# Kernel tuning notes

Measured on AMD Instinct MI355X. Metric: run time of the kernel, lower is better.

## Reference

```python
import jax, jax.numpy as jnp
import numpy as np

STRIDE = 16
A = 9
PRE_NMS_TOP_N = 6000
POST_NMS_TOP_N = 300
NMS_THRESH = 0.7
MIN_SIZE = 16
H, W = 128, 192


def _generate_anchors(base_size=16, ratios=(0.5, 1.0, 2.0), scales=(8, 16, 32)):
    base = np.array([0, 0, base_size - 1, base_size - 1], dtype=np.float64)
    w = base[2] - base[0] + 1
    h = base[3] - base[1] + 1
    x_ctr = base[0] + 0.5 * (w - 1)
    y_ctr = base[1] + 0.5 * (h - 1)
    size = w * h
    ratios = np.array(ratios)
    ws = np.round(np.sqrt(size / ratios))
    hs = np.round(ws * ratios)
    ratio_anchors = np.stack([x_ctr - 0.5 * (ws - 1), y_ctr - 0.5 * (hs - 1),
                              x_ctr + 0.5 * (ws - 1), y_ctr + 0.5 * (hs - 1)], axis=1)
    out = []
    scales = np.array(scales)
    for a in ratio_anchors:
        aw = a[2] - a[0] + 1
        ah = a[3] - a[1] + 1
        xc = a[0] + 0.5 * (aw - 1)
        yc = a[1] + 0.5 * (ah - 1)
        ws2 = aw * scales
        hs2 = ah * scales
        out.append(np.stack([xc - 0.5 * (ws2 - 1), yc - 0.5 * (hs2 - 1),
                             xc + 0.5 * (ws2 - 1), yc + 0.5 * (hs2 - 1)], axis=1))
    return np.concatenate(out, axis=0).astype(np.float32)  # [9,4]


def setup_inputs() -> dict:
    key = jax.random.key(0)
    k1, k2 = jax.random.split(key)
    scores = jax.random.uniform(k1, (1, 2 * A, H, W), dtype=jnp.float32)
    bbox_deltas = 0.1 * jax.random.normal(k2, (1, 4 * A, H, W), dtype=jnp.float32)
    im_info = jnp.array([[H * STRIDE, W * STRIDE, 1.0]], dtype=jnp.float32)
    return {"scores": scores, "bbox_deltas": bbox_deltas, "im_info": im_info}


def _proposal_forward(scores, bbox_deltas, im_info):
    anchors_base = jnp.asarray(_generate_anchors())  # [A,4]
    sc = scores[:, A:, :, :]                          # fg scores [1,A,H,W]
    h, w = sc.shape[-2], sc.shape[-1]
    shift_x = (jnp.arange(w) * STRIDE).astype(sc.dtype)
    shift_y = (jnp.arange(h) * STRIDE).astype(sc.dtype)
    sy, sx = jnp.meshgrid(shift_y, shift_x, indexing='ij')
    shifts = jnp.stack([sx.ravel(), sy.ravel(), sx.ravel(), sy.ravel()], axis=1)  # [K,4]
    anchors = (anchors_base[None, :, :] + shifts[:, None, :]).reshape(-1, 4)      # [K*A,4]

    deltas = bbox_deltas.transpose(0, 2, 3, 1).reshape(-1, 4)
    deltas = jnp.concatenate([deltas[:, :2], jnp.clip(deltas[:, 2:], -10.0, 10.0)], axis=1)
    sc = sc.transpose(0, 2, 3, 1).reshape(-1)  # [K*A]

    widths = anchors[:, 2] - anchors[:, 0] + 1.0
    heights = anchors[:, 3] - anchors[:, 1] + 1.0
    ctr_x = anchors[:, 0] + 0.5 * widths
    ctr_y = anchors[:, 1] + 0.5 * heights
    dx, dy, dw, dh = deltas[:, 0], deltas[:, 1], deltas[:, 2], deltas[:, 3]
    pcx = dx * widths + ctr_x
    pcy = dy * heights + ctr_y
    pw = jnp.exp(dw) * widths
    ph = jnp.exp(dh) * heights
    x1 = pcx - 0.5 * pw
    y1 = pcy - 0.5 * ph
    x2 = pcx + 0.5 * pw
    y2 = pcy + 0.5 * ph

    info = im_info[0]
    x1 = jnp.clip(x1, 0.0, info[1] - 1.0)
    x2 = jnp.clip(x2, 0.0, info[1] - 1.0)
    y1 = jnp.clip(y1, 0.0, info[0] - 1.0)
    y2 = jnp.clip(y2, 0.0, info[0] - 1.0)
    proposals = jnp.stack([x1, y1, x2, y2], axis=1)

    # filter_boxes: mask (instead of dropping) boxes smaller than min_size*scale
    min_sz = MIN_SIZE * info[2]
    valid = ((x2 - x1 + 1.0) >= min_sz) & ((y2 - y1 + 1.0) >= min_sz)
    masked = jnp.where(valid, sc, -jnp.inf)

    # sort desc + pre_nms_topN
    top_scores, top_idx = jax.lax.top_k(masked, PRE_NMS_TOP_N)
    boxes = proposals[top_idx]               # [PRE,4], score-descending
    tvalid = top_scores > -jnp.inf

    # pairwise IoU (torchvision convention)
    area = (boxes[:, 2] - boxes[:, 0]) * (boxes[:, 3] - boxes[:, 1])
    lt = jnp.maximum(boxes[:, None, :2], boxes[None, :, :2])
    rb = jnp.minimum(boxes[:, None, 2:], boxes[None, :, 2:])
    wh = jnp.clip(rb - lt, 0.0)
    inter = wh[..., 0] * wh[..., 1]
    iou = inter / (area[:, None] + area[None, :] - inter)  # [PRE,PRE]

    # greedy NMS over score-sorted boxes
    n = PRE_NMS_TOP_N
    def step(keep, x):
        iou_col, v, i = x
        suppressed = jnp.any(keep & (iou_col > NMS_THRESH))
        k = v & jnp.logical_not(suppressed)
        keep = keep.at[i].set(k)
        return keep, k
    keep, _ = jax.lax.scan(step, jnp.zeros((n,), dtype=bool),
                           (iou.T, tvalid, jnp.arange(n)))

    # kept boxes first (stable => score order preserved), take post_nms_topN
    order = jnp.argsort(jnp.logical_not(keep).astype(jnp.int32), stable=True)[:POST_NMS_TOP_N]
    kept = keep[order]
    out_boxes = jnp.where(kept[:, None], boxes[order], 0.0)
    output = jnp.concatenate(
        [jnp.zeros((POST_NMS_TOP_N, 1), out_boxes.dtype), out_boxes], axis=1)
    return output  # [POST,5]: (batch_idx=0, x1,y1,x2,y2); rows beyond kept count are zero


def reference(scores, bbox_deltas, im_info):
    return _proposal_forward(scores, bbox_deltas, im_info)
```

## Files before the change

### kernel.cpp

```cpp
#include <hip/hip_runtime.h>

#define N_ANCH 221184
#define HW     24576
#define Wd     192
#define AA     9
#define TOPN   6000
#define POSTN  300
#define CAND_CAP 8192
#define NWORDS 94
#define NCHUNK 47

typedef unsigned long long u64;

__device__ const float c_aw[9] = {184.f,368.f,736.f,128.f,256.f,512.f, 88.f,176.f,352.f};
__device__ const float c_ah[9] = { 96.f,192.f,384.f,128.f,256.f,512.f,176.f,352.f,704.f};

__device__ __forceinline__ float4 decode_box(int a, int cell,
                                             const float* __restrict__ deltas,
                                             float info0, float info1, float info2,
                                             bool* valid) {
    int h = cell / Wd;
    int w = cell - h * Wd;
    const float* db = deltas + (size_t)(4 * a) * HW + cell;
    float dx = db[0];
    float dy = db[HW];
    float dw = db[2 * HW];
    float dh = db[3 * HW];
    dw = fminf(fmaxf(dw, -10.f), 10.f);
    dh = fminf(fmaxf(dh, -10.f), 10.f);

    float ww = c_aw[a], hh = c_ah[a];
    float cx = 16.f * (float)w + 8.f;
    float cy = 16.f * (float)h + 8.f;

    float pcx = __fadd_rn(__fmul_rn(dx, ww), cx);
    float pcy = __fadd_rn(__fmul_rn(dy, hh), cy);
    float pw  = __fmul_rn(expf(dw), ww);
    float ph  = __fmul_rn(expf(dh), hh);
    float hpw = __fmul_rn(0.5f, pw);
    float hph = __fmul_rn(0.5f, ph);
    float x1 = __fsub_rn(pcx, hpw);
    float x2 = __fadd_rn(pcx, hpw);
    float y1 = __fsub_rn(pcy, hph);
    float y2 = __fadd_rn(pcy, hph);

    float xmax = __fsub_rn(info1, 1.f);
    float ymax = __fsub_rn(info0, 1.f);
    x1 = fminf(fmaxf(x1, 0.f), xmax);
    x2 = fminf(fmaxf(x2, 0.f), xmax);
    y1 = fminf(fmaxf(y1, 0.f), ymax);
    y2 = fminf(fmaxf(y2, 0.f), ymax);

    float msz = __fmul_rn(16.f, info2);
    *valid = (__fadd_rn(__fsub_rn(x2, x1), 1.f) >= msz) &&
             (__fadd_rn(__fsub_rn(y2, y1), 1.f) >= msz);
    return make_float4(x1, y1, x2, y2);
}

#define ZA_F4 4164
#define ZB_F4 48
__global__ __launch_bounds__(256) void init_kernel(float4* zA, float4* zB) {
    int t = blockIdx.x * 256 + threadIdx.x;
    float4 z = make_float4(0.f, 0.f, 0.f, 0.f);
    if (t < ZA_F4) zA[t] = z;
    else if (t < ZA_F4 + ZB_F4) zB[t - ZA_F4] = z;
}

__global__ __launch_bounds__(256) void decode_kernel(const float* __restrict__ scores,
                                                     const float* __restrict__ deltas,
                                                     const float* __restrict__ iminfo,
                                                     unsigned int* __restrict__ keys,
                                                     unsigned int* __restrict__ hist256) {
    __shared__ unsigned int lh[256];
    lh[threadIdx.x] = 0u;
    __syncthreads();
    int t = blockIdx.x * 256 + threadIdx.x;
    int a = t / HW;
    int cell = t - a * HW;
    float score = scores[(AA + a) * HW + cell];
    bool valid;
    (void)decode_box(a, cell, deltas, iminfo[0], iminfo[1], iminfo[2], &valid);
    unsigned int sb = __float_as_uint(score);
    unsigned int key = valid ? ((sb & 0x80000000u) ? ~sb : (sb | 0x80000000u))
                             : 0x007FFFFFu;
    keys[t] = key;
    atomicAdd(&lh[key >> 24], 1u);
    __syncthreads();
    if (lh[threadIdx.x]) atomicAdd(&hist256[threadIdx.x], lh[threadIdx.x]);
}

__global__ __launch_bounds__(1024) void midselect_kernel(const unsigned int* __restrict__ keys,
                                                         const unsigned int* __restrict__ hist256,
                                                         unsigned int* __restrict__ state) {
    __shared__ unsigned int sfx[256];
    __shared__ unsigned int h2w[16][256];
    __shared__ unsigned int sP, sRank;
    int t = threadIdx.x;
    int wv = t >> 6;
    for (int i = t; i < 16 * 256; i += 1024) ((unsigned int*)h2w)[i] = 0u;
    if (t < 256) sfx[t] = hist256[t];
    __syncthreads();
    for (int d = 1; d < 256; d <<= 1) {
        unsigned int v = 0u;
        if (t < 256 && t + d < 256) v = sfx[t + d];
        __syncthreads();
        if (t < 256) sfx[t] += v;
        __syncthreads();
    }
    if (t < 256) {
        unsigned int ge = sfx[t];
        unsigned int gt = (t < 255) ? sfx[t + 1] : 0u;
        if (ge >= TOPN && gt < TOPN) { sP = (unsigned int)t; sRank = TOPN - gt; }
    }
    __syncthreads();
    unsigned int P = sP, rank = sRank;
    const uint4* k4 = (const uint4*)keys;
    for (int i = t; i < N_ANCH / 4; i += 1024) {
        uint4 v = k4[i];
        if ((v.x >> 24) == P) atomicAdd(&h2w[wv][(v.x >> 16) & 0xFFu], 1u);
        if ((v.y >> 24) == P) atomicAdd(&h2w[wv][(v.y >> 16) & 0xFFu], 1u);
        if ((v.z >> 24) == P) atomicAdd(&h2w[wv][(v.z >> 16) & 0xFFu], 1u);
        if ((v.w >> 24) == P) atomicAdd(&h2w[wv][(v.w >> 16) & 0xFFu], 1u);
    }
    __syncthreads();
    if (t < 256) {
        unsigned int s = 0;
        #pragma unroll
        for (int wvi = 0; wvi < 16; ++wvi) s += h2w[wvi][t];
        sfx[t] = s;
    }
    __syncthreads();
    for (int d = 1; d < 256; d <<= 1) {
        unsigned int v = 0u;
        if (t < 256 && t + d < 256) v = sfx[t + d];
        __syncthreads();
        if (t < 256) sfx[t] += v;
        __syncthreads();
    }
    if (t < 256) {
        unsigned int ge = sfx[t];
        unsigned int gt = (t < 255) ? sfx[t + 1] : 0u;
        if (ge >= rank && gt < rank) {
            state[0] = (P << 24) | ((unsigned int)t << 16);
            state[2] = 0u;
        }
    }
}

__global__ __launch_bounds__(256) void compact_kernel(const unsigned int* __restrict__ keys,
                                                      unsigned int* __restrict__ state,
                                                      u64* __restrict__ cand) {
    int t = blockIdx.x * 256 + threadIdx.x;
    unsigned int k = keys[t];
    unsigned int T = state[0];
    if (k >= T) {
        unsigned int pos = atomicAdd(&state[2], 1u);
        if (pos < CAND_CAP) {
            int a = t / HW;
            int cell = t - a * HW;
            unsigned int aidx = (unsigned int)(cell * 9 + a);
            cand[pos] = ((u64)k << 32) | (u64)(~aidx);
        }
    }
}

__global__ __launch_bounds__(256) void rank_scatter_kernel(const u64* __restrict__ cand,
                                                           const float* __restrict__ deltas,
                                                           const float* __restrict__ iminfo,
                                                           float4* __restrict__ tb,
                                                           u64* __restrict__ vmask) {
    __shared__ u64 s[CAND_CAP];
    for (int j = threadIdx.x; j < CAND_CAP; j += 256) s[j] = cand[j];
    int part = threadIdx.x & 7;
    int i = blockIdx.x * 32 + (threadIdx.x >> 3);
    u64 k = cand[i];
    __syncthreads();
    const ulonglong2* sv = (const ulonglong2*)s;
    unsigned int cnt = 0;
    #pragma unroll 8
    for (int jj = part; jj < CAND_CAP / 2; jj += 8) {
        ulonglong2 v = sv[jj];
        cnt += (v.x > k) ? 1u : 0u;
        cnt += (v.y > k) ? 1u : 0u;
    }
    cnt += __shfl_xor(cnt, 1);
    cnt += __shfl_xor(cnt, 2);
    cnt += __shfl_xor(cnt, 4);
    if (part == 0 && k != 0ull && cnt < TOPN) {
        unsigned int aidx = ~((unsigned int)k);
        int a = (int)(aidx % 9u);
        int cell = (int)(aidx / 9u);
        bool valid;
        float4 box = decode_box(a, cell, deltas, iminfo[0], iminfo[1], iminfo[2], &valid);
        tb[cnt] = box;
        if ((unsigned int)(k >> 32) != 0x007FFFFFu)
            atomicOr(&vmask[cnt >> 6], 1ull << (cnt & 63));
    }
}

__global__ __launch_bounds__(64) void nms_matrix_kernel(const float4* __restrict__ tb,
                                                        u64* __restrict__ mat) {
    if (blockIdx.x < blockIdx.y) return;
    __shared__ float4 cb[64];
    int t = threadIdx.x;
    int c0 = blockIdx.x * 64;
    int col = c0 + t;
    cb[t] = (col < TOPN) ? tb[col] : make_float4(0.f, 0.f, 0.f, 0.f);
    __syncthreads();
    int row = blockIdx.y * 64 + t;
    if (row >= TOPN) return;
    float4 rb = tb[row];
    float rA = (rb.z - rb.x) * (rb.w - rb.y);
    u64 mask = 0ull;
    for (int c = 0; c < 64; ++c) {
        if (c0 + c >= TOPN) break;
        float4 b = cb[c];
        float lx = fmaxf(rb.x, b.x), ly = fmaxf(rb.y, b.y);
        float rx = fminf(rb.z, b.z), ry = fminf(rb.w, b.w);
        float iw = fmaxf(rx - lx, 0.f), ih = fmaxf(ry - ly, 0.f);
        float inter = iw * ih;
        float bA = (b.z - b.x) * (b.w - b.y);
        float iou = inter / ((rA + bA) - inter);
        if (iou > 0.7f) mask |= (1ull << c);
    }
    mat[(size_t)row * NWORDS + blockIdx.x] = mask;
}

__device__ __forceinline__ u64 rdl64(u64 v, int l) {
    unsigned int lo = (unsigned int)__builtin_amdgcn_readlane((int)(unsigned int)v, l);
    unsigned int hi = (unsigned int)__builtin_amdgcn_readlane((int)(unsigned int)(v >> 32), l);
    return ((u64)hi << 32) | (u64)lo;
}

__global__ __launch_bounds__(64) void nms_scan_kernel(const u64* __restrict__ mat,
                                                      const u64* __restrict__ vmask,
                                                      const float4* __restrict__ tb,
                                                      float* __restrict__ out) {
    int lane = threadIdx.x;
    u64 r0 = ~vmask[lane];
    u64 r1 = (lane < NWORDS - 64) ? ~vmask[64 + lane] : ~0ull;
    __shared__ int kept[POSTN];
    int cnt = 0;

    u64 a0, a1, b0, b1;
    {
        ulonglong2 vA = *(const ulonglong2*)(mat + (size_t)lane * NWORDS);
        ulonglong2 vB = *(const ulonglong2*)(mat + (size_t)(64 + lane) * NWORDS);
        a0 = vA.x; a1 = vA.y; b0 = vB.x; b1 = vB.y;
    }
    for (int c = 0; c < NCHUNK; ++c) {
        u64 na0 = 0, na1 = 0, nb0 = 0, nb1 = 0;
        if (c + 1 < NCHUNK) {
            const u64* pA = mat + (size_t)((c + 1) * 128 + lane) * NWORDS + 2 * (c + 1);
            const u64* pB = mat + (size_t)((c + 1) * 128 + 64 + lane) * NWORDS + 2 * (c + 1);
            ulonglong2 vA = *(const ulonglong2*)pA;
            ulonglong2 vB = *(const ulonglong2*)pB;
            na0 = vA.x; na1 = vA.y; nb0 = vB.x; nb1 = vB.y;
        }
        int w2 = 2 * c;
        u64 s0 = (w2 < 64) ? rdl64(r0, w2) : rdl64(r1, w2 - 64);
        u64 s1 = (w2 + 1 < 64) ? rdl64(r0, w2 + 1) : rdl64(r1, w2 + 1 - 64);
        if ((s0 & s1) != ~0ull) {
            int base = c * 128;
            u64 rem0 = s0, rem1 = s1, k0 = 0ull, k1 = 0ull;
            while (cnt < POSTN) {
                int b;
                if (~rem0) b = __ffsll((u64)~rem0) - 1;
                else if (~rem1) b = 64 + __ffsll((u64)~rem1) - 1;
                else break;
                if (lane == 0) kept[cnt] = base + b;
                ++cnt;
                u64 w0, w1;
                if (b < 64) {
                    w0 = rdl64(a0, b); w1 = rdl64(a1, b);
                    k0 |= 1ull << b; rem0 |= 1ull << b;
                } else {
                    int bb = b - 64;
                    w0 = rdl64(b0, bb); w1 = rdl64(b1, bb);
                    k1 |= 1ull << bb; rem1 |= 1ull << bb;
                }
                rem0 |= w0; rem1 |= w1;
            }
            if (cnt >= POSTN) break;
            u64 f0 = 0ull, f1 = 0ull, m0 = k0, m1 = k1;
            while (m0 | m1) {
                int idxs[8];
                #pragma unroll
                for (int j = 0; j < 8; ++j) {
                    int b = -1;
                    if (m0) { b = __ffsll(m0) - 1; m0 &= m0 - 1; }
                    else if (m1) { b = 64 + __ffsll(m1) - 1; m1 &= m1 - 1; }
                    idxs[j] = b;
                }
                u64 v0[8], v1[8];
                #pragma unroll
                for (int j = 0; j < 8; ++j) {
                    v0[j] = 0ull; v1[j] = 0ull;
                    if (idxs[j] >= 0) {
                        const u64* row = mat + (size_t)(base + idxs[j]) * NWORDS;
                        v0[j] = row[lane];
                        if (lane < NWORDS - 64) v1[j] = row[64 + lane];
                    }
                }
                #pragma unroll
                for (int j = 0; j < 8; ++j) { f0 |= v0[j]; f1 |= v1[j]; }
            }
            r0 |= f0; r1 |= f1;
        }
        a0 = na0; a1 = na1; b0 = nb0; b1 = nb1;
    }

    for (int r = lane; r < POSTN; r += 64) {
        float4 b = make_float4(0.f, 0.f, 0.f, 0.f);
        if (r < cnt) b = tb[kept[r]];
        float* o = out + r * 5;
        o[0] = 0.f; o[1] = b.x; o[2] = b.y; o[3] = b.z; o[4] = b.w;
    }
}

extern "C" void kernel_launch(void* const* d_in, const int* in_sizes, int n_in,
                              void* d_out, int out_size, void* d_ws, size_t ws_size,
                              hipStream_t stream) {
    const float* scores = (const float*)d_in[0];
    const float* deltas = (const float*)d_in[1];
    const float* iminfo = (const float*)d_in[2];
    float* out = (float*)d_out;

    char* ws = (char*)d_ws;
    unsigned int* keys    = (unsigned int*)(ws + 0);
    unsigned int* hist256 = (unsigned int*)(ws + 884736);
    unsigned int* state   = (unsigned int*)(ws + 885760);
    u64*          cand    = (u64*)(ws + 885824);
    float4*       tb      = (float4*)(ws + 951360);
    u64*          vmask   = (u64*)(ws + 1047616);
    u64*          mat     = (u64*)(ws + 1048384);

    const int NB = N_ANCH / 256;

    init_kernel<<<17, 256, 0, stream>>>((float4*)hist256, (float4*)vmask);
    decode_kernel<<<NB, 256, 0, stream>>>(scores, deltas, iminfo, keys, hist256);
    midselect_kernel<<<1, 1024, 0, stream>>>(keys, hist256, state);
    compact_kernel<<<NB, 256, 0, stream>>>(keys, state, cand);
    rank_scatter_kernel<<<CAND_CAP / 32, 256, 0, stream>>>(cand, deltas, iminfo, tb, vmask);
    nms_matrix_kernel<<<dim3(NWORDS, NWORDS), 64, 0, stream>>>(tb, mat);
    nms_scan_kernel<<<1, 64, 0, stream>>>(mat, vmask, tb, out);
}
```

Before: 249.1 us.

## Speculatively prefetch next chunk's suppression rows and deepen diagonal-block prefetch

The serial NMS scan now prefetches the diagonal mask blocks four chunks ahead instead of one. While processing a chunk, it also speculatively loads up to eight mask rows for the next chunk's currently-unsuppressed candidates, so the dependent global loads overlap with the current chunk's work. When the kept boxes of a chunk match the speculated rows, the prefetched data is reused and only uncovered rows are fetched. This costs extra register pressure and some wasted loads when speculation misses, in exchange for hiding memory latency on the single-wavefront critical path.

```diff
diff --git a/kernel.cpp b/kernel.cpp
--- a/kernel.cpp
+++ b/kernel.cpp
@@ -232,6 +232,126 @@
     return ((u64)hi << 32) | (u64)lo;
 }
 
+struct Spec {
+    u64 v0[8];
+    u64 v1[8];
+    u64 m0, m1;
+};
+
+__device__ __forceinline__ bool chunk_body(int c, int lane,
+                                           const u64* __restrict__ mat,
+                                           ulonglong2 dA, ulonglong2 dB,
+                                           Spec& in, Spec& out,
+                                           u64& r0, u64& r1, int& cnt,
+                                           int* kept) {
+    const int w2 = 2 * c;
+    u64 s0 = (w2 < 64) ? rdl64(r0, w2) : rdl64(r1, w2 - 64);
+    u64 s1 = (w2 + 1 < 64) ? rdl64(r0, w2 + 1) : rdl64(r1, w2 + 1 - 64);
+
+    {
+        const int cn = (c + 1 < NCHUNK) ? (c + 1) : (NCHUNK - 1);
+        const int w2n = 2 * cn;
+        u64 t0 = (w2n < 64) ? rdl64(r0, w2n) : rdl64(r1, w2n - 64);
+        u64 t1 = (w2n + 1 < 64) ? rdl64(r0, w2n + 1) : rdl64(r1, w2n + 1 - 64);
+        u64 p0 = ~t0, p1 = ~t1;
+        out.m0 = p0; out.m1 = p1;
+        const int nbase = cn * 128;
+        const u64 lmask = (lane < NWORDS - 64) ? ~0ull : 0ull;
+        const int l1 = (lane < NWORDS - 64) ? (64 + lane) : 63;
+        u64 mm0 = p0, mm1 = p1;
+        #pragma unroll
+        for (int j = 0; j < 8; ++j) {
+            int b = -1;
+            if (mm0)      { b = __ffsll(mm0) - 1;      mm0 &= mm0 - 1; }
+            else if (mm1) { b = 64 + __ffsll(mm1) - 1; mm1 &= mm1 - 1; }
+            int bS = (b >= 0) ? b : 0;
+            const u64* row = mat + (size_t)(nbase + bS) * NWORDS;
+            u64 x0 = row[lane];
+            u64 x1 = row[l1];
+            u64 live = (b >= 0) ? ~0ull : 0ull;
+            out.v0[j] = x0 & live;
+            out.v1[j] = x1 & live & lmask;
+        }
+    }
+
+    if ((s0 & s1) != ~0ull) {
+        const int base = c * 128;
+        u64 rem0 = s0, rem1 = s1, k0 = 0ull, k1 = 0ull;
+        while (cnt < POSTN) {
+            int b;
+            if (~rem0)      b = __ffsll((u64)~rem0) - 1;
+            else if (~rem1) b = 64 + __ffsll((u64)~rem1) - 1;
+            else break;
+            if (lane == 0) kept[cnt] = base + b;
+            ++cnt;
+            if (b < 64) {
+                rem0 |= rdl64(dA.x, b);
+                rem1 |= rdl64(dA.y, b);
+                k0 |= 1ull << b; rem0 |= 1ull << b;
+            } else {
+                int bb = b - 64;
+                rem0 |= rdl64(dB.x, bb);
+                rem1 |= rdl64(dB.y, bb);
+                k1 |= 1ull << bb; rem1 |= 1ull << bb;
+            }
+        }
+        if (cnt >= POSTN) return true;
+
+        if (k0 | k1) {
+            u64 mm0 = in.m0, mm1 = in.m1, cov0 = 0ull, cov1 = 0ull;
+            u64 f0 = 0ull, f1 = 0ull;
+            #pragma unroll
+            for (int j = 0; j < 8; ++j) {
+                int b = -1;
+                if (mm0)      { b = __ffsll(mm0) - 1;      mm0 &= mm0 - 1; }
+                else if (mm1) { b = 64 + __ffsll(mm1) - 1; mm1 &= mm1 - 1; }
+                if (b >= 0) {
+                    u64 kj;
+                    if (b < 64) { kj = (k0 >> b) & 1ull;        cov0 |= 1ull << b; }
+                    else        { kj = (k1 >> (b - 64)) & 1ull; cov1 |= 1ull << (b - 64); }
+                    u64 msk = 0ull - kj;
+                    f0 |= in.v0[j] & msk;
+                    f1 |= in.v1[j] & msk;
+                }
+            }
+            u64 lk0 = k0 & ~cov0, lk1 = k1 & ~cov1;
+            if (lk0 | lk1) {
+                u64 m0 = lk0, m1 = lk1;
+                while (m0 | m1) {
+                    int idxs[8];
+                    #pragma unroll
+                    for (int j = 0; j < 8; ++j) {
+                        int b = -1;
+                        if (m0)      { b = __ffsll(m0) - 1;      m0 &= m0 - 1; }
+                        else if (m1) { b = 64 + __ffsll(m1) - 1; m1 &= m1 - 1; }
+                        idxs[j] = b;
+                    }
+                    u64 v0[8], v1[8];
+                    #pragma unroll
+                    for (int j = 0; j < 8; ++j) {
+                        v0[j] = 0ull; v1[j] = 0ull;
+                        if (idxs[j] >= 0) {
+                            const u64* row = mat + (size_t)(base + idxs[j]) * NWORDS;
+                            v0[j] = row[lane];
+                            if (lane < NWORDS - 64) v1[j] = row[64 + lane];
+                        }
+                    }
+                    #pragma unroll
+                    for (int j = 0; j < 8; ++j) { f0 |= v0[j]; f1 |= v1[j]; }
+                }
+            }
+            r0 |= f0; r1 |= f1;
+        }
+    }
+    return false;
+}
+
+#define LDIAG(cc, A, B) do {                                                  \
+    int c_ = (cc) < NCHUNK ? (cc) : (NCHUNK - 1);                             \
+    const u64* pA_ = mat + (size_t)(c_ * 128 + lane) * NWORDS + 2 * c_;       \
+    const u64* pB_ = mat + (size_t)(c_ * 128 + 64 + lane) * NWORDS + 2 * c_;  \
+    A = *(const ulonglong2*)pA_; B = *(const ulonglong2*)pB_; } while (0)
+
 __global__ __launch_bounds__(64) void nms_scan_kernel(const u64* __restrict__ mat,
                                                       const u64* __restrict__ vmask,
                                                       const float4* __restrict__ tb,
@@ -242,72 +362,34 @@
     __shared__ int kept[POSTN];
     int cnt = 0;
 
-    u64 a0, a1, b0, b1;
-    {
-        ulonglong2 vA = *(const ulonglong2*)(mat + (size_t)lane * NWORDS);
-        ulonglong2 vB = *(const ulonglong2*)(mat + (size_t)(64 + lane) * NWORDS);
-        a0 = vA.x; a1 = vA.y; b0 = vB.x; b1 = vB.y;
-    }
-    for (int c = 0; c < NCHUNK; ++c) {
-        u64 na0 = 0, na1 = 0, nb0 = 0, nb1 = 0;
-        if (c + 1 < NCHUNK) {
-            const u64* pA = mat + (size_t)((c + 1) * 128 + lane) * NWORDS + 2 * (c + 1);
-            const u64* pB = mat + (size_t)((c + 1) * 128 + 64 + lane) * NWORDS + 2 * (c + 1);
-            ulonglong2 vA = *(const ulonglong2*)pA;
-            ulonglong2 vB = *(const ulonglong2*)pB;
-            na0 = vA.x; na1 = vA.y; nb0 = vB.x; nb1 = vB.y;
-        }
-        int w2 = 2 * c;
-        u64 s0 = (w2 < 64) ? rdl64(r0, w2) : rdl64(r1, w2 - 64);
-        u64 s1 = (w2 + 1 < 64) ? rdl64(r0, w2 + 1) : rdl64(r1, w2 + 1 - 64);
-        if ((s0 & s1) != ~0ull) {
-            int base = c * 128;
-            u64 rem0 = s0, rem1 = s1, k0 = 0ull, k1 = 0ull;
-            while (cnt < POSTN) {
-                int b;
-                if (~rem0) b = __ffsll((u64)~rem0) - 1;
-                else if (~rem1) b = 64 + __ffsll((u64)~rem1) - 1;
-                else break;
-                if (lane == 0) kept[cnt] = base + b;
-                ++cnt;
-                u64 w0, w1;
-                if (b < 64) {
-                    w0 = rdl64(a0, b); w1 = rdl64(a1, b);
-                    k0 |= 1ull << b; rem0 |= 1ull << b;
-                } else {
-                    int bb = b - 64;
-                    w0 = rdl64(b0, bb); w1 = rdl64(b1, bb);
-                    k1 |= 1ull << bb; rem1 |= 1ull << bb;
-                }
-                rem0 |= w0; rem1 |= w1;
-            }
-            if (cnt >= POSTN) break;
-            u64 f0 = 0ull, f1 = 0ull, m0 = k0, m1 = k1;
-            while (m0 | m1) {
-                int idxs[8];
-                #pragma unroll
-                for (int j = 0; j < 8; ++j) {
-                    int b = -1;
-                    if (m0) { b = __ffsll(m0) - 1; m0 &= m0 - 1; }
-                    else if (m1) { b = 64 + __ffsll(m1) - 1; m1 &= m1 - 1; }
-                    idxs[j] = b;
-                }
-                u64 v0[8], v1[8];
-                #pragma unroll
-                for (int j = 0; j < 8; ++j) {
-                    v0[j] = 0ull; v1[j] = 0ull;
-                    if (idxs[j] >= 0) {
-                        const u64* row = mat + (size_t)(base + idxs[j]) * NWORDS;
-                        v0[j] = row[lane];
-                        if (lane < NWORDS - 64) v1[j] = row[64 + lane];
-                    }
-                }
-                #pragma unroll
-                for (int j = 0; j < 8; ++j) { f0 |= v0[j]; f1 |= v1[j]; }
-            }
-            r0 |= f0; r1 |= f1;
-        }
-        a0 = na0; a1 = na1; b0 = nb0; b1 = nb1;
+    ulonglong2 z2; z2.x = 0ull; z2.y = 0ull;
+    ulonglong2 cA0, cB0, cA1, cB1, cA2, cB2, cA3, cB3;
+    LDIAG(0, cA0, cB0); LDIAG(1, cA1, cB1);
+    LDIAG(2, cA2, cB2); LDIAG(3, cA3, cB3);
+
+    Spec S0, S1;
+    S0.m0 = S0.m1 = 0ull; S1.m0 = S1.m1 = 0ull;
+    #pragma unroll
+    for (int j = 0; j < 8; ++j) { S0.v0[j] = S0.v1[j] = S1.v0[j] = S1.v1[j] = 0ull; }
+
+    bool done = false;
+    for (int g = 0; g < 12 && !done; ++g) {
+        int cb = g * 4;
+        ulonglong2 nA0 = z2, nB0 = z2, nA1 = z2, nB1 = z2;
+        ulonglong2 nA2 = z2, nB2 = z2, nA3 = z2, nB3 = z2;
+        LDIAG(cb + 4, nA0, nB0); LDIAG(cb + 5, nA1, nB1);
+        LDIAG(cb + 6, nA2, nB2); LDIAG(cb + 7, nA3, nB3);
+
+        done = chunk_body(cb, lane, mat, cA0, cB0, S0, S1, r0, r1, cnt, kept);
+        if (!done && cb + 1 < NCHUNK)
+            done = chunk_body(cb + 1, lane, mat, cA1, cB1, S1, S0, r0, r1, cnt, kept);
+        if (!done && cb + 2 < NCHUNK)
+            done = chunk_body(cb + 2, lane, mat, cA2, cB2, S0, S1, r0, r1, cnt, kept);
+        if (!done && cb + 3 < NCHUNK)
+            done = chunk_body(cb + 3, lane, mat, cA3, cB3, S1, S0, r0, r1, cnt, kept);
+
+        cA0 = nA0; cB0 = nB0; cA1 = nA1; cB1 = nB1;
+        cA2 = nA2; cB2 = nB2; cA3 = nA3; cB3 = nB3;
     }
 
     for (int r = lane; r < POSTN; r += 64) {
```

After: 267.5 us. 7.4% more time.

## Software-pipeline NMS scan by deferring suppression-row ORs one chunk

Applied to the files above, without the earlier changes.

The serial NMS scan now loads each chunk's diagonal block together with the next block's columns. The next chunk's suppression state can then be formed from those words without waiting for the kept rows' global loads. Up to eight kept-row loads per chunk are issued and their OR is deferred to the following chunk, so load latency overlaps with the next chunk's greedy loop. Chunks are processed in ping-pong pairs. This adds register pressure and more complex control flow, and kept rows beyond the first eight are still loaded synchronously.

```diff
diff --git a/kernel.cpp b/kernel.cpp
--- a/kernel.cpp
+++ b/kernel.cpp
@@ -232,6 +232,101 @@
     return ((u64)hi << 32) | (u64)lo;
 }
 
+struct DiagX { ulonglong2 a, ax, b, bx; };
+struct Pend { u64 v0[8], v1[8], lm[8]; };
+
+__device__ __forceinline__ bool chunk_body(int c, int lane,
+                                           const u64* __restrict__ mat,
+                                           const DiagX& D, Pend& in, Pend& out,
+                                           u64& s0, u64& s1,
+                                           u64& r0, u64& r1, int& cnt, int* kept,
+                                           const u64 lmask, const int l1) {
+    const int base = c * 128;
+    u64 k0 = 0ull, k1 = 0ull, nx0 = 0ull, nx1 = 0ull;
+
+    if ((s0 & s1) != ~0ull) {
+        u64 rem0 = s0, rem1 = s1;
+        while (cnt < POSTN) {
+            int b;
+            if (~rem0)      b = __ffsll((u64)~rem0) - 1;
+            else if (~rem1) b = 64 + __ffsll((u64)~rem1) - 1;
+            else break;
+            if (lane == 0) kept[cnt] = base + b;
+            ++cnt;
+            if (b < 64) {
+                rem0 |= rdl64(D.a.x, b);
+                rem1 |= rdl64(D.a.y, b);
+                nx0  |= rdl64(D.ax.x, b);
+                nx1  |= rdl64(D.ax.y, b);
+                k0 |= 1ull << b; rem0 |= 1ull << b;
+            } else {
+                int bb = b - 64;
+                rem0 |= rdl64(D.b.x, bb);
+                rem1 |= rdl64(D.b.y, bb);
+                nx0  |= rdl64(D.bx.x, bb);
+                nx1  |= rdl64(D.bx.y, bb);
+                k1 |= 1ull << bb; rem1 |= 1ull << bb;
+            }
+        }
+        if (cnt >= POSTN) return true;
+    }
+
+    {
+        u64 m0 = k0, m1 = k1;
+        #pragma unroll
+        for (int j = 0; j < 8; ++j) {
+            int b = -1;
+            if (m0)      { b = __ffsll(m0) - 1;      m0 &= m0 - 1; }
+            else if (m1) { b = 64 + __ffsll(m1) - 1; m1 &= m1 - 1; }
+            int bS = (b >= 0) ? b : 0;
+            const u64* row = mat + (size_t)(base + bS) * NWORDS;
+            out.v0[j] = row[lane];
+            out.v1[j] = row[l1];
+            out.lm[j] = (b >= 0) ? ~0ull : 0ull;
+        }
+        while (m0 | m1) {
+            int b;
+            if (m0) { b = __ffsll(m0) - 1; m0 &= m0 - 1; }
+            else    { b = 64 + __ffsll(m1) - 1; m1 &= m1 - 1; }
+            const u64* row = mat + (size_t)(base + b) * NWORDS;
+            r0 |= row[lane];
+            if (lane < NWORDS - 64) r1 |= row[64 + lane];
+        }
+    }
+
+    {
+        u64 f0 = 0ull, f1 = 0ull;
+        #pragma unroll
+        for (int j = 0; j < 8; ++j) {
+            f0 |= in.v0[j] & in.lm[j];
+            f1 |= in.v1[j] & in.lm[j];
+        }
+        r0 |= f0;
+        r1 |= f1 & lmask;
+    }
+
+    {
+        int w = 2 * c + 2;
+        u64 t0, t1;
+        if (w < 64) { t0 = rdl64(r0, w);      t1 = rdl64(r0, w + 1); }
+        else        { t0 = rdl64(r1, w - 64); t1 = rdl64(r1, w - 63); }
+        s0 = t0 | nx0;
+        s1 = t1 | nx1;
+    }
+    return false;
+}
+
+#define LDIAGX(cc, D) do {                                                    \
+    int c_ = (cc) < NCHUNK ? (cc) : (NCHUNK - 1);                             \
+    const u64* pA_ = mat + (size_t)(c_ * 128 + lane) * NWORDS + 2 * c_;       \
+    const u64* pB_ = mat + (size_t)(c_ * 128 + 64 + lane) * NWORDS + 2 * c_;  \
+    int xo_ = (2 * c_ + 3 < NWORDS) ? 2 : 0;                                  \
+    (D).a  = *(const ulonglong2*)pA_;                                         \
+    (D).ax = *(const ulonglong2*)(pA_ + xo_);                                 \
+    (D).b  = *(const ulonglong2*)pB_;                                         \
+    (D).bx = *(const ulonglong2*)(pB_ + xo_);                                 \
+} while (0)
+
 __global__ __launch_bounds__(64) void nms_scan_kernel(const u64* __restrict__ mat,
                                                       const u64* __restrict__ vmask,
                                                       const float4* __restrict__ tb,
@@ -241,73 +336,34 @@
     u64 r1 = (lane < NWORDS - 64) ? ~vmask[64 + lane] : ~0ull;
     __shared__ int kept[POSTN];
     int cnt = 0;
-
-    u64 a0, a1, b0, b1;
-    {
-        ulonglong2 vA = *(const ulonglong2*)(mat + (size_t)lane * NWORDS);
-        ulonglong2 vB = *(const ulonglong2*)(mat + (size_t)(64 + lane) * NWORDS);
-        a0 = vA.x; a1 = vA.y; b0 = vB.x; b1 = vB.y;
-    }
-    for (int c = 0; c < NCHUNK; ++c) {
-        u64 na0 = 0, na1 = 0, nb0 = 0, nb1 = 0;
-        if (c + 1 < NCHUNK) {
-            const u64* pA = mat + (size_t)((c + 1) * 128 + lane) * NWORDS + 2 * (c + 1);
-            const u64* pB = mat + (size_t)((c + 1) * 128 + 64 + lane) * NWORDS + 2 * (c + 1);
-            ulonglong2 vA = *(const ulonglong2*)pA;
-            ulonglong2 vB = *(const ulonglong2*)pB;
-            na0 = vA.x; na1 = vA.y; nb0 = vB.x; nb1 = vB.y;
-        }
-        int w2 = 2 * c;
-        u64 s0 = (w2 < 64) ? rdl64(r0, w2) : rdl64(r1, w2 - 64);
-        u64 s1 = (w2 + 1 < 64) ? rdl64(r0, w2 + 1) : rdl64(r1, w2 + 1 - 64);
-        if ((s0 & s1) != ~0ull) {
-            int base = c * 128;
-            u64 rem0 = s0, rem1 = s1, k0 = 0ull, k1 = 0ull;
-            while (cnt < POSTN) {
-                int b;
-                if (~rem0) b = __ffsll((u64)~rem0) - 1;
-                else if (~rem1) b = 64 + __ffsll((u64)~rem1) - 1;
-                else break;
-                if (lane == 0) kept[cnt] = base + b;
-                ++cnt;
-                u64 w0, w1;
-                if (b < 64) {
-                    w0 = rdl64(a0, b); w1 = rdl64(a1, b);
-                    k0 |= 1ull << b; rem0 |= 1ull << b;
-                } else {
-                    int bb = b - 64;
-                    w0 = rdl64(b0, bb); w1 = rdl64(b1, bb);
-                    k1 |= 1ull << bb; rem1 |= 1ull << bb;
-                }
-                rem0 |= w0; rem1 |= w1;
-            }
-            if (cnt >= POSTN) break;
-            u64 f0 = 0ull, f1 = 0ull, m0 = k0, m1 = k1;
-            while (m0 | m1) {
-                int idxs[8];
-                #pragma unroll
-                for (int j = 0; j < 8; ++j) {
-                    int b = -1;
-                    if (m0) { b = __ffsll(m0) - 1; m0 &= m0 - 1; }
-                    else if (m1) { b = 64 + __ffsll(m1) - 1; m1 &= m1 - 1; }
-                    idxs[j] = b;
-                }
-                u64 v0[8], v1[8];
-                #pragma unroll
-                for (int j = 0; j < 8; ++j) {
-                    v0[j] = 0ull; v1[j] = 0ull;
-                    if (idxs[j] >= 0) {
-                        const u64* row = mat + (size_t)(base + idxs[j]) * NWORDS;
-                        v0[j] = row[lane];
-                        if (lane < NWORDS - 64) v1[j] = row[64 + lane];
-                    }
-                }
-                #pragma unroll
-                for (int j = 0; j < 8; ++j) { f0 |= v0[j]; f1 |= v1[j]; }
-            }
-            r0 |= f0; r1 |= f1;
-        }
-        a0 = na0; a1 = na1; b0 = nb0; b1 = nb1;
+    const u64 lmask = (lane < NWORDS - 64) ? ~0ull : 0ull;
+    const int l1 = (lane < NWORDS - 64) ? (64 + lane) : 63;
+
+    Pend PA, PB;
+    #pragma unroll
+    for (int j = 0; j < 8; ++j) {
+        PA.v0[j] = PA.v1[j] = PA.lm[j] = 0ull;
+        PB.v0[j] = PB.v1[j] = PB.lm[j] = 0ull;
+    }
+
+    DiagX Da, Db, Dn;
+    LDIAGX(0, Da);
+    u64 s0 = rdl64(r0, 0);
+    u64 s1 = rdl64(r0, 1);
+
+    bool done = false;
+    for (int p = 0; p < (NCHUNK + 1) / 2 && !done; ++p) {
+        int c0 = 2 * p, c1 = 2 * p + 1;
+        LDIAGX(c1, Db);
+        done = chunk_body(c0, lane, mat, Da, PA, PB, s0, s1, r0, r1, cnt, kept,
+                          lmask, l1);
+        if (done) break;
+        LDIAGX(c1 + 1, Dn);
+        if (c1 < NCHUNK) {
+            done = chunk_body(c1, lane, mat, Db, PB, PA, s0, s1, r0, r1, cnt,
+                              kept, lmask, l1);
+        }
+        Da = Dn;
     }
 
     for (int r = lane; r < POSTN; r += 64) {
```

Result: slower. 330.3 us (+32.6%).

## Build 16-bit key histogram in decode to drop the single-block key rescan

Applied to the files above, without the earlier changes.

The decode kernel now does a global atomic increment into a 65536-bin histogram indexed by the top 16 bits of each key. The midselect kernel then reads the 256 bins under the selected top byte instead of rescanning all keys with one workgroup, and shrinks to 256 threads. The init kernel grows to zero the new histogram, which reuses the NMS matrix workspace region. The trade is one extra global atomic per anchor, and with uniform scores these atomics pile onto a small set of bins, so contention can offset the removed serial scan.

```diff
diff --git a/kernel.cpp b/kernel.cpp
--- a/kernel.cpp
+++ b/kernel.cpp
@@ -59,18 +59,22 @@
 
 #define ZA_F4 4164
 #define ZB_F4 48
-__global__ __launch_bounds__(256) void init_kernel(float4* zA, float4* zB) {
+#define ZC_F4 16384
+__global__ __launch_bounds__(256) void init_kernel(float4* zA, float4* zB,
+                                                   float4* zC) {
     int t = blockIdx.x * 256 + threadIdx.x;
     float4 z = make_float4(0.f, 0.f, 0.f, 0.f);
     if (t < ZA_F4) zA[t] = z;
     else if (t < ZA_F4 + ZB_F4) zB[t - ZA_F4] = z;
+    else if (t < ZA_F4 + ZB_F4 + ZC_F4) zC[t - ZA_F4 - ZB_F4] = z;
 }
 
 __global__ __launch_bounds__(256) void decode_kernel(const float* __restrict__ scores,
                                                      const float* __restrict__ deltas,
                                                      const float* __restrict__ iminfo,
                                                      unsigned int* __restrict__ keys,
-                                                     unsigned int* __restrict__ hist256) {
+                                                     unsigned int* __restrict__ hist256,
+                                                     unsigned int* __restrict__ hist64k) {
     __shared__ unsigned int lh[256];
     lh[threadIdx.x] = 0u;
     __syncthreads();
@@ -84,66 +88,46 @@
     unsigned int key = valid ? ((sb & 0x80000000u) ? ~sb : (sb | 0x80000000u))
                              : 0x007FFFFFu;
     keys[t] = key;
+    atomicAdd(&hist64k[key >> 16], 1u);
     atomicAdd(&lh[key >> 24], 1u);
     __syncthreads();
     if (lh[threadIdx.x]) atomicAdd(&hist256[threadIdx.x], lh[threadIdx.x]);
 }
 
-__global__ __launch_bounds__(1024) void midselect_kernel(const unsigned int* __restrict__ keys,
-                                                         const unsigned int* __restrict__ hist256,
-                                                         unsigned int* __restrict__ state) {
+__global__ __launch_bounds__(256) void midselect_kernel(const unsigned int* __restrict__ hist256,
+                                                        const unsigned int* __restrict__ hist64k,
+                                                        unsigned int* __restrict__ state) {
     __shared__ unsigned int sfx[256];
-    __shared__ unsigned int h2w[16][256];
     __shared__ unsigned int sP, sRank;
     int t = threadIdx.x;
-    int wv = t >> 6;
-    for (int i = t; i < 16 * 256; i += 1024) ((unsigned int*)h2w)[i] = 0u;
-    if (t < 256) sfx[t] = hist256[t];
+    sfx[t] = hist256[t];
     __syncthreads();
     for (int d = 1; d < 256; d <<= 1) {
-        unsigned int v = 0u;
-        if (t < 256 && t + d < 256) v = sfx[t + d];
+        unsigned int v = (t + d < 256) ? sfx[t + d] : 0u;
         __syncthreads();
-        if (t < 256) sfx[t] += v;
+        sfx[t] += v;
         __syncthreads();
     }
-    if (t < 256) {
+    {
         unsigned int ge = sfx[t];
         unsigned int gt = (t < 255) ? sfx[t + 1] : 0u;
         if (ge >= TOPN && gt < TOPN) { sP = (unsigned int)t; sRank = TOPN - gt; }
     }
     __syncthreads();
     unsigned int P = sP, rank = sRank;
-    const uint4* k4 = (const uint4*)keys;
-    for (int i = t; i < N_ANCH / 4; i += 1024) {
-        uint4 v = k4[i];
-        if ((v.x >> 24) == P) atomicAdd(&h2w[wv][(v.x >> 16) & 0xFFu], 1u);
-        if ((v.y >> 24) == P) atomicAdd(&h2w[wv][(v.y >> 16) & 0xFFu], 1u);
-        if ((v.z >> 24) == P) atomicAdd(&h2w[wv][(v.z >> 16) & 0xFFu], 1u);
-        if ((v.w >> 24) == P) atomicAdd(&h2w[wv][(v.w >> 16) & 0xFFu], 1u);
-    }
-    __syncthreads();
-    if (t < 256) {
-        unsigned int s = 0;
-        #pragma unroll
-        for (int wvi = 0; wvi < 16; ++wvi) s += h2w[wvi][t];
-        sfx[t] = s;
-    }
+    sfx[t] = hist64k[(P << 8) + (unsigned int)t];
     __syncthreads();
     for (int d = 1; d < 256; d <<= 1) {
-        unsigned int v = 0u;
-        if (t < 256 && t + d < 256) v = sfx[t + d];
+        unsigned int v = (t + d < 256) ? sfx[t + d] : 0u;
         __syncthreads();
-        if (t < 256) sfx[t] += v;
+        sfx[t] += v;
         __syncthreads();
     }
-    if (t < 256) {
+    {
         unsigned int ge = sfx[t];
         unsigned int gt = (t < 255) ? sfx[t + 1] : 0u;
-        if (ge >= rank && gt < rank) {
+        if (ge >= rank && gt < rank)
             state[0] = (P << 24) | ((unsigned int)t << 16);
-            state[2] = 0u;
-        }
     }
 }
 
@@ -334,12 +318,15 @@
     float4*       tb      = (float4*)(ws + 951360);
     u64*          vmask   = (u64*)(ws + 1047616);
     u64*          mat     = (u64*)(ws + 1048384);
+    unsigned int* hist64k = (unsigned int*)(ws + 1048384);
 
     const int NB = N_ANCH / 256;
 
-    init_kernel<<<17, 256, 0, stream>>>((float4*)hist256, (float4*)vmask);
-    decode_kernel<<<NB, 256, 0, stream>>>(scores, deltas, iminfo, keys, hist256);
-    midselect_kernel<<<1, 1024, 0, stream>>>(keys, hist256, state);
+    init_kernel<<<81, 256, 0, stream>>>((float4*)hist256, (float4*)vmask,
+                                        (float4*)hist64k);
+    decode_kernel<<<NB, 256, 0, stream>>>(scores, deltas, iminfo, keys,
+                                          hist256, hist64k);
+    midselect_kernel<<<1, 256, 0, stream>>>(hist256, hist64k, state);
     compact_kernel<<<NB, 256, 0, stream>>>(keys, state, cand);
     rank_scatter_kernel<<<CAND_CAP / 32, 256, 0, stream>>>(cand, deltas, iminfo, tb, vmask);
     nms_matrix_kernel<<<dim3(NWORDS, NWORDS), 64, 0, stream>>>(tb, mat);
```

Result: slower. 315.2 us (+26.5%).
